# Optimization experiments

Measured on AMD Instinct MI355X. Metric: run time of the kernel, lower is better.

Reference implementation:

```python
import jax, jax.numpy as jnp
import numpy as np

D = 6          # atom_dims, fixed by GroupNorm(2, D) and reshape(-1, 6)
K = 16         # neighbors
N_LAYERS = 3
C_IN = 2 * D + 1  # 13
EPS = 1e-5
SLOPE = 0.2


def _lrelu(x):
    return jnp.where(x >= 0, x, SLOPE * x)


def _group_norm(x, w, b):
    # x: [M, D], 2 groups of D//2 channels, affine per channel
    m = x.shape[0]
    xg = x.reshape(m, 2, D // 2)
    mu = xg.mean(-1, keepdims=True)
    var = xg.var(-1, keepdims=True)
    xn = ((xg - mu) * jax.lax.rsqrt(var + EPS)).reshape(m, D)
    return xn * w + b


def setup_inputs() -> dict:
    key = jax.random.key(0)
    ks = jax.random.split(key, 8)
    B, N = 4, 100000
    dist = jax.random.uniform(ks[0], (B, N, K, 1), dtype=jnp.float32)
    atomtypes = jax.random.uniform(ks[1], (B, N, K, D), dtype=jnp.float32)
    s1 = 1.0 / np.sqrt(C_IN)
    W1 = jax.random.uniform(ks[2], (N_LAYERS, C_IN, C_IN), jnp.float32, -s1, s1)
    b1 = jax.random.uniform(ks[3], (N_LAYERS, C_IN), jnp.float32, -s1, s1)
    W2 = jax.random.uniform(ks[4], (N_LAYERS, C_IN, D), jnp.float32, -s1, s1)
    b2 = jax.random.uniform(ks[5], (N_LAYERS, D), jnp.float32, -s1, s1)
    gw = jnp.ones((N_LAYERS, D), jnp.float32)
    gb = jnp.zeros((N_LAYERS, D), jnp.float32)
    return {"dist": dist, "atomtypes": atomtypes, "W1": W1, "b1": b1,
            "W2": W2, "b2": b2, "gw": gw, "gb": gb}


def reference(dist, atomtypes, W1, b1, W2, b2, gw, gb):
    B, N, k, d = atomtypes.shape
    point_emb = jnp.ones((B, N, d), dtype=atomtypes.dtype)
    for i in range(N_LAYERS):
        # [B,N,k,2D+1]: broadcast point emb to neighbors, concat atom feats + dist
        feat = jnp.concatenate(
            [jnp.broadcast_to(point_emb[:, :, None, :], (B, N, k, d)),
             atomtypes, dist], axis=-1)
        h = _lrelu(jnp.einsum('bnkc,cd->bnkd', feat, W1[i]) + b1[i])
        msg = (jnp.einsum('bnkc,cd->bnkd', h, W2[i]) + b2[i]).sum(-2)  # [B,N,D]
        upd = _lrelu(_group_norm(msg.reshape(-1, d), gw[i], gb[i])).reshape(B, N, d)
        point_emb = point_emb + upd
    return point_emb
```

## Files before the change

kernel.cpp:

```cpp
#include <hip/hip_runtime.h>


constexpr int DD  = 6;
constexpr int KK  = 16;
constexpr int CIN = 13;
constexpr float EPSV = 1e-5f;

__global__ __launch_bounds__(256) void atom_mp(
    const float* __restrict__ dist,
    const float* __restrict__ at,
    const float* __restrict__ W1,
    const float* __restrict__ b1,
    const float* __restrict__ W2,
    const float* __restrict__ b2,
    const float* __restrict__ gw,
    const float* __restrict__ gb,
    float* __restrict__ out,
    int P)
{
    int t = blockIdx.x * blockDim.x + threadIdx.x;
    int p = t >> 1;
    int h = t & 1;
    if (p >= P) return;

    float a[8 * DD];
    float dq[8];

    const float4* ap4 = reinterpret_cast<const float4*>(
        at + (long)p * (KK * DD) + h * (8 * DD));
    #pragma unroll
    for (int i = 0; i < 12; ++i) {
        float4 q = ap4[i];
        a[4 * i + 0] = q.x; a[4 * i + 1] = q.y;
        a[4 * i + 2] = q.z; a[4 * i + 3] = q.w;
    }
    const float4* dp4 = reinterpret_cast<const float4*>(
        dist + (long)p * KK + h * 8);
    #pragma unroll
    for (int i = 0; i < 2; ++i) {
        float4 q = dp4[i];
        dq[4 * i + 0] = q.x; dq[4 * i + 1] = q.y;
        dq[4 * i + 2] = q.z; dq[4 * i + 3] = q.w;
    }

    float pe[DD] = {1.f, 1.f, 1.f, 1.f, 1.f, 1.f};

    #pragma unroll 1
    for (int L = 0; L < 3; ++L) {
        const float* w1  = W1 + L * CIN * CIN;
        const float* w2  = W2 + L * CIN * DD;
        const float* bb1 = b1 + L * CIN;
        const float* bb2 = b2 + L * DD;
        const float* gwp = gw + L * DD;
        const float* gbp = gb + L * DD;

        float hsum[CIN];

        #pragma unroll
        for (int d = 0; d < CIN; ++d) {
            float s = bb1[d];
            #pragma unroll
            for (int c = 0; c < DD; ++c)
                s = fmaf(pe[c], w1[c * CIN + d], s);

            float w0 = w1[6 * CIN + d];
            float acc[8];
            #pragma unroll
            for (int k = 0; k < 8; ++k)
                acc[k] = fmaf(a[6 * k + 0], w0, s);
            #pragma unroll
            for (int j = 1; j < 7; ++j) {
                float w = w1[(6 + j) * CIN + d];
                #pragma unroll
                for (int k = 0; k < 8; ++k) {
                    float fv = (j < 6) ? a[6 * k + j] : dq[k];
                    acc[k] = fmaf(fv, w, acc[k]);
                }
            }
            float hs = 0.f;
            #pragma unroll
            for (int k = 0; k < 8; ++k) {
                hs = fmaf(0.6f, acc[k], hs);
                hs = fmaf(0.4f, __builtin_fabsf(acc[k]), hs);
            }
            hsum[d] = hs;
        }

        #pragma unroll
        for (int d = 0; d < CIN; ++d)
            hsum[d] += __shfl_xor(hsum[d], 1, 64);

        float msg[DD];
        #pragma unroll
        for (int d = 0; d < DD; ++d) {
            float m = 16.f * bb2[d];
            #pragma unroll
            for (int c = 0; c < CIN; ++c)
                m = fmaf(hsum[c], w2[c * DD + d], m);
            msg[d] = m;
        }

        #pragma unroll
        for (int g = 0; g < 2; ++g) {
            float m0 = msg[3 * g], m1 = msg[3 * g + 1], m2 = msg[3 * g + 2];
            float mu = (m0 + m1 + m2) * (1.f / 3.f);
            float d0 = m0 - mu, d1 = m1 - mu, d2 = m2 - mu;
            float var = (d0 * d0 + d1 * d1 + d2 * d2) * (1.f / 3.f);
            float rs = rsqrtf(var + EPSV);
            float dv[3] = {d0, d1, d2};
            #pragma unroll
            for (int c = 0; c < 3; ++c) {
                int ch = 3 * g + c;
                float xn = fmaf(dv[c] * rs, gwp[ch], gbp[ch]);
                pe[ch] = fmaf(0.6f, xn, pe[ch]);
                pe[ch] = fmaf(0.4f, __builtin_fabsf(xn), pe[ch]);
            }
        }
    }

    float* op = out + (long)p * DD;
    if (h == 0) {
        *reinterpret_cast<float2*>(op)     = make_float2(pe[0], pe[1]);
        *reinterpret_cast<float2*>(op + 2) = make_float2(pe[2], pe[3]);
    } else {
        *reinterpret_cast<float2*>(op + 4) = make_float2(pe[4], pe[5]);
    }
}

extern "C" void kernel_launch(void* const* d_in, const int* in_sizes, int n_in,
                              void* d_out, int out_size, void* d_ws, size_t ws_size,
                              hipStream_t stream) {
    const float* dist = (const float*)d_in[0];
    const float* at   = (const float*)d_in[1];
    const float* W1   = (const float*)d_in[2];
    const float* b1   = (const float*)d_in[3];
    const float* W2   = (const float*)d_in[4];
    const float* b2   = (const float*)d_in[5];
    const float* gw   = (const float*)d_in[6];
    const float* gb   = (const float*)d_in[7];
    float* out = (float*)d_out;

    int P = in_sizes[0] / KK;
    long threads_total = 2L * P;
    int threads = 256;
    int blocks = (int)((threads_total + threads - 1) / threads);
    atom_mp<<<blocks, threads, 0, stream>>>(dist, at, W1, b1, W2, b2, gw, gb, out, P);
}
```

Before: 272.7 us.

## Use packed FP32 FMAs and hoist linear part of leaky-ReLU sum

```diff
diff --git a/kernel.cpp b/kernel.cpp
--- a/kernel.cpp
+++ b/kernel.cpp
@@ -1,12 +1,19 @@
 #include <hip/hip_runtime.h>
 
+
+typedef float f2 __attribute__((ext_vector_type(2)));
 
 constexpr int DD  = 6;
 constexpr int KK  = 16;
 constexpr int CIN = 13;
 constexpr float EPSV = 1e-5f;
 
-__global__ __launch_bounds__(256) void atom_mp(
+__device__ __forceinline__ f2 pkfma(f2 a, f2 b, f2 c) {
+    return __builtin_elementwise_fma(a, b, c);
+}
+__device__ __forceinline__ f2 splat(float x) { f2 r; r.x = x; r.y = x; return r; }
+
+__global__ __launch_bounds__(256, 3) void atom_mp(
     const float* __restrict__ dist,
     const float* __restrict__ at,
     const float* __restrict__ W1,
@@ -25,7 +32,6 @@
 
     float a[8 * DD];
     float dq[8];
-
     const float4* ap4 = reinterpret_cast<const float4*>(
         at + (long)p * (KK * DD) + h * (8 * DD));
     #pragma unroll
@@ -34,13 +40,27 @@
         a[4 * i + 0] = q.x; a[4 * i + 1] = q.y;
         a[4 * i + 2] = q.z; a[4 * i + 3] = q.w;
     }
-    const float4* dp4 = reinterpret_cast<const float4*>(
-        dist + (long)p * KK + h * 8);
+    const float4* dp4 = reinterpret_cast<const float4*>(dist + (long)p * KK + h * 8);
     #pragma unroll
     for (int i = 0; i < 2; ++i) {
         float4 q = dp4[i];
         dq[4 * i + 0] = q.x; dq[4 * i + 1] = q.y;
         dq[4 * i + 2] = q.z; dq[4 * i + 3] = q.w;
+    }
+
+    float S[7];
+    #pragma unroll
+    for (int j = 0; j < 6; ++j) {
+        float s = a[j];
+        #pragma unroll
+        for (int k = 1; k < 8; ++k) s += a[6 * k + j];
+        S[j] = s;
+    }
+    {
+        float s = dq[0];
+        #pragma unroll
+        for (int k = 1; k < 8; ++k) s += dq[k];
+        S[6] = s;
     }
 
     float pe[DD] = {1.f, 1.f, 1.f, 1.f, 1.f, 1.f};
@@ -54,51 +74,109 @@
         const float* gwp = gw + L * DD;
         const float* gbp = gb + L * DD;
 
+        f2 base2[6];
+        float base_s;
+        #pragma unroll
+        for (int dp = 0; dp < 6; ++dp) {
+            f2 b = {bb1[2 * dp], bb1[2 * dp + 1]};
+            #pragma unroll
+            for (int c = 0; c < 6; ++c) {
+                f2 w = {w1[c * CIN + 2 * dp], w1[c * CIN + 2 * dp + 1]};
+                b = pkfma(splat(pe[c]), w, b);
+            }
+            base2[dp] = b;
+        }
+        base_s = bb1[12];
+        #pragma unroll
+        for (int c = 0; c < 6; ++c)
+            base_s = fmaf(pe[c], w1[c * CIN + 12], base_s);
+
+        f2 lin2[6];
+        float lin_s;
+        #pragma unroll
+        for (int dp = 0; dp < 6; ++dp) {
+            f2 l = base2[dp] * splat(8.f);
+            #pragma unroll
+            for (int j = 0; j < 7; ++j) {
+                f2 w = {w1[(6 + j) * CIN + 2 * dp], w1[(6 + j) * CIN + 2 * dp + 1]};
+                l = pkfma(splat(S[j]), w, l);
+            }
+            lin2[dp] = l;
+        }
+        lin_s = 8.f * base_s;
+        #pragma unroll
+        for (int j = 0; j < 7; ++j)
+            lin_s = fmaf(S[j], w1[(6 + j) * CIN + 12], lin_s);
+
+        float habs[CIN];
+        #pragma unroll
+        for (int d = 0; d < CIN; ++d) habs[d] = 0.f;
+
+        #pragma unroll
+        for (int k = 0; k < 8; ++k) {
+            f2 acc2[6];
+            float acc_s;
+            {
+                float f0 = a[6 * k];
+                f2 fv = splat(f0);
+                #pragma unroll
+                for (int dp = 0; dp < 6; ++dp) {
+                    f2 w = {w1[6 * CIN + 2 * dp], w1[6 * CIN + 2 * dp + 1]};
+                    acc2[dp] = pkfma(fv, w, base2[dp]);
+                }
+                acc_s = fmaf(f0, w1[6 * CIN + 12], base_s);
+            }
+            #pragma unroll
+            for (int j = 1; j < 6; ++j) {
+                float fj = a[6 * k + j];
+                f2 fv = splat(fj);
+                #pragma unroll
+                for (int dp = 0; dp < 6; ++dp) {
+                    f2 w = {w1[(6 + j) * CIN + 2 * dp], w1[(6 + j) * CIN + 2 * dp + 1]};
+                    acc2[dp] = pkfma(fv, w, acc2[dp]);
+                }
+                acc_s = fmaf(fj, w1[(6 + j) * CIN + 12], acc_s);
+            }
+            {
+                float fj = dq[k];
+                f2 fv = splat(fj);
+                #pragma unroll
+                for (int dp = 0; dp < 6; ++dp) {
+                    f2 w = {w1[12 * CIN + 2 * dp], w1[12 * CIN + 2 * dp + 1]};
+                    acc2[dp] = pkfma(fv, w, acc2[dp]);
+                }
+                acc_s = fmaf(fj, w1[12 * CIN + 12], acc_s);
+            }
+            #pragma unroll
+            for (int dp = 0; dp < 6; ++dp) {
+                habs[2 * dp]     += __builtin_fabsf(acc2[dp].x);
+                habs[2 * dp + 1] += __builtin_fabsf(acc2[dp].y);
+            }
+            habs[12] += __builtin_fabsf(acc_s);
+        }
+
         float hsum[CIN];
-
         #pragma unroll
         for (int d = 0; d < CIN; ++d) {
-            float s = bb1[d];
-            #pragma unroll
-            for (int c = 0; c < DD; ++c)
-                s = fmaf(pe[c], w1[c * CIN + d], s);
-
-            float w0 = w1[6 * CIN + d];
-            float acc[8];
-            #pragma unroll
-            for (int k = 0; k < 8; ++k)
-                acc[k] = fmaf(a[6 * k + 0], w0, s);
-            #pragma unroll
-            for (int j = 1; j < 7; ++j) {
-                float w = w1[(6 + j) * CIN + d];
-                #pragma unroll
-                for (int k = 0; k < 8; ++k) {
-                    float fv = (j < 6) ? a[6 * k + j] : dq[k];
-                    acc[k] = fmaf(fv, w, acc[k]);
-                }
-            }
-            float hs = 0.f;
-            #pragma unroll
-            for (int k = 0; k < 8; ++k) {
-                hs = fmaf(0.6f, acc[k], hs);
-                hs = fmaf(0.4f, __builtin_fabsf(acc[k]), hs);
-            }
-            hsum[d] = hs;
-        }
-
-        #pragma unroll
-        for (int d = 0; d < CIN; ++d)
-            hsum[d] += __shfl_xor(hsum[d], 1, 64);
-
-        float msg[DD];
-        #pragma unroll
-        for (int d = 0; d < DD; ++d) {
-            float m = 16.f * bb2[d];
-            #pragma unroll
-            for (int c = 0; c < CIN; ++c)
-                m = fmaf(hsum[c], w2[c * DD + d], m);
-            msg[d] = m;
-        }
+            float lin_d = (d < 12) ? ((d & 1) ? lin2[d >> 1].y : lin2[d >> 1].x)
+                                   : lin_s;
+            float v = fmaf(0.6f, lin_d, 0.4f * habs[d]);
+            hsum[d] = v + __shfl_xor(v, 1, 64);
+        }
+
+        f2 msg2[3];
+        #pragma unroll
+        for (int dp = 0; dp < 3; ++dp) {
+            f2 m = {16.f * bb2[2 * dp], 16.f * bb2[2 * dp + 1]};
+            #pragma unroll
+            for (int c = 0; c < CIN; ++c) {
+                f2 w = {w2[c * DD + 2 * dp], w2[c * DD + 2 * dp + 1]};
+                m = pkfma(splat(hsum[c]), w, m);
+            }
+            msg2[dp] = m;
+        }
+        float msg[DD] = {msg2[0].x, msg2[0].y, msg2[1].x, msg2[1].y,
+                         msg2[2].x, msg2[2].y};
 
         #pragma unroll
         for (int g = 0; g < 2; ++g) {
```

After: 405.3 us. 48.6% more time.

## Stream neighbor features from memory per layer instead of holding them in registers

Applied to the files above, without the earlier changes.

```diff
diff --git a/kernel.cpp b/kernel.cpp
--- a/kernel.cpp
+++ b/kernel.cpp
@@ -6,7 +6,7 @@
 constexpr int CIN = 13;
 constexpr float EPSV = 1e-5f;
 
-__global__ __launch_bounds__(256) void atom_mp(
+__global__ __launch_bounds__(256, 6) void atom_mp(
     const float* __restrict__ dist,
     const float* __restrict__ at,
     const float* __restrict__ W1,
@@ -18,30 +18,13 @@
     float* __restrict__ out,
     int P)
 {
-    int t = blockIdx.x * blockDim.x + threadIdx.x;
+    int t = blockIdx.x * 256 + threadIdx.x;
     int p = t >> 1;
     int h = t & 1;
     if (p >= P) return;
 
-    float a[8 * DD];
-    float dq[8];
-
-    const float4* ap4 = reinterpret_cast<const float4*>(
-        at + (long)p * (KK * DD) + h * (8 * DD));
-    #pragma unroll
-    for (int i = 0; i < 12; ++i) {
-        float4 q = ap4[i];
-        a[4 * i + 0] = q.x; a[4 * i + 1] = q.y;
-        a[4 * i + 2] = q.z; a[4 * i + 3] = q.w;
-    }
-    const float4* dp4 = reinterpret_cast<const float4*>(
-        dist + (long)p * KK + h * 8);
-    #pragma unroll
-    for (int i = 0; i < 2; ++i) {
-        float4 q = dp4[i];
-        dq[4 * i + 0] = q.x; dq[4 * i + 1] = q.y;
-        dq[4 * i + 2] = q.z; dq[4 * i + 3] = q.w;
-    }
+    const float* fa = at   + (long)p * (KK * DD) + h * 48;
+    const float* fd = dist + (long)p * KK + h * 8;
 
     float pe[DD] = {1.f, 1.f, 1.f, 1.f, 1.f, 1.f};
 
@@ -54,36 +37,96 @@
         const float* gwp = gw + L * DD;
         const float* gbp = gb + L * DD;
 
-        float hsum[CIN];
-
+        float base[CIN];
         #pragma unroll
         for (int d = 0; d < CIN; ++d) {
             float s = bb1[d];
             #pragma unroll
             for (int c = 0; c < DD; ++c)
                 s = fmaf(pe[c], w1[c * CIN + d], s);
+            base[d] = s;
+        }
 
-            float w0 = w1[6 * CIN + d];
-            float acc[8];
+        float hsum[CIN];
+
+        {
+            float wv[7][7];
             #pragma unroll
-            for (int k = 0; k < 8; ++k)
-                acc[k] = fmaf(a[6 * k + 0], w0, s);
+            for (int j = 0; j < 7; ++j)
+                #pragma unroll
+                for (int d = 0; d < 7; ++d)
+                    wv[j][d] = w1[(6 + j) * CIN + d];
+
+            float hs[7] = {0.f, 0.f, 0.f, 0.f, 0.f, 0.f, 0.f};
+
             #pragma unroll
-            for (int j = 1; j < 7; ++j) {
-                float w = w1[(6 + j) * CIN + d];
+            for (int kp = 0; kp < 4; ++kp) {
+                float4 q0 = *reinterpret_cast<const float4*>(fa + kp * 12);
+                float4 q1 = *reinterpret_cast<const float4*>(fa + kp * 12 + 4);
+                float4 q2 = *reinterpret_cast<const float4*>(fa + kp * 12 + 8);
+                float2 dq = *reinterpret_cast<const float2*>(fd + kp * 2);
+                float f0[7] = {q0.x, q0.y, q0.z, q0.w, q1.x, q1.y, dq.x};
+                float f1[7] = {q1.z, q1.w, q2.x, q2.y, q2.z, q2.w, dq.y};
+
                 #pragma unroll
-                for (int k = 0; k < 8; ++k) {
-                    float fv = (j < 6) ? a[6 * k + j] : dq[k];
-                    acc[k] = fmaf(fv, w, acc[k]);
+                for (int d = 0; d < 7; ++d) {
+                    float x0 = base[d];
+                    float x1 = base[d];
+                    #pragma unroll
+                    for (int j = 0; j < 7; ++j) {
+                        x0 = fmaf(f0[j], wv[j][d], x0);
+                        x1 = fmaf(f1[j], wv[j][d], x1);
+                    }
+                    float s = hs[d];
+                    s = fmaf(0.6f, x0, s);
+                    s = fmaf(0.4f, __builtin_fabsf(x0), s);
+                    s = fmaf(0.6f, x1, s);
+                    s = fmaf(0.4f, __builtin_fabsf(x1), s);
+                    hs[d] = s;
                 }
             }
-            float hs = 0.f;
             #pragma unroll
-            for (int k = 0; k < 8; ++k) {
-                hs = fmaf(0.6f, acc[k], hs);
-                hs = fmaf(0.4f, __builtin_fabsf(acc[k]), hs);
+            for (int d = 0; d < 7; ++d) hsum[d] = hs[d];
+        }
+
+        {
+            float wv[7][6];
+            #pragma unroll
+            for (int j = 0; j < 7; ++j)
+                #pragma unroll
+                for (int d = 0; d < 6; ++d)
+                    wv[j][d] = w1[(6 + j) * CIN + 7 + d];
+
+            float hs[6] = {0.f, 0.f, 0.f, 0.f, 0.f, 0.f};
+
+            #pragma unroll
+            for (int kp = 0; kp < 4; ++kp) {
+                float4 q0 = *reinterpret_cast<const float4*>(fa + kp * 12);
+                float4 q1 = *reinterpret_cast<const float4*>(fa + kp * 12 + 4);
+                float4 q2 = *reinterpret_cast<const float4*>(fa + kp * 12 + 8);
+                float2 dq = *reinterpret_cast<const float2*>(fd + kp * 2);
+                float f0[7] = {q0.x, q0.y, q0.z, q0.w, q1.x, q1.y, dq.x};
+                float f1[7] = {q1.z, q1.w, q2.x, q2.y, q2.z, q2.w, dq.y};
+
+                #pragma unroll
+                for (int d = 0; d < 6; ++d) {
+                    float x0 = base[7 + d];
+                    float x1 = base[7 + d];
+                    #pragma unroll
+                    for (int j = 0; j < 7; ++j) {
+                        x0 = fmaf(f0[j], wv[j][d], x0);
+                        x1 = fmaf(f1[j], wv[j][d], x1);
+                    }
+                    float s = hs[d];
+                    s = fmaf(0.6f, x0, s);
+                    s = fmaf(0.4f, __builtin_fabsf(x0), s);
+                    s = fmaf(0.6f, x1, s);
+                    s = fmaf(0.4f, __builtin_fabsf(x1), s);
+                    hs[d] = s;
+                }
             }
-            hsum[d] = hs;
+            #pragma unroll
+            for (int d = 0; d < 6; ++d) hsum[7 + d] = hs[d];
         }
 
         #pragma unroll
@@ -142,7 +185,6 @@
 
     int P = in_sizes[0] / KK;
     long threads_total = 2L * P;
-    int threads = 256;
-    int blocks = (int)((threads_total + threads - 1) / threads);
-    atom_mp<<<blocks, threads, 0, stream>>>(dist, at, W1, b1, W2, b2, gw, gb, out, P);
+    int blocks = (int)((threads_total + 255) / 256);
+    atom_mp<<<blocks, 256, 0, stream>>>(dist, at, W1, b1, W2, b2, gw, gb, out, P);
 }
```

Result: slower. 507.5 us (+86.1%).
